# Kernel optimization log

Measured on AMD Instinct MI355X. Metric: run time of the kernel, lower is better.

## Reference

```python
import jax, jax.numpy as jnp
import numpy as np

NUM_RBF = 16
TOP_K = 30
MAXREL = 32  # max_relative_feature
M_CTX = 16   # ligand context atoms per residue

PT_GROUP = jnp.array([0,1,18,1,2,13,14,15,16,17,18,1,2,13,14,15,16,17,18,1,2,3,4,5,6,7,8,9,10,11,12,13,14,15,16,17,18,1,2,3,4,5,6,7,8,9,10,11,12,13,14,15,16,17,18,1,2,3,3,3,3,3,3,3,3,3,3,3,3,3,3,3,4,5,6,7,8,9,10,11,12,13,14,15,16,17,18,1,2,3,3,3,3,3,3,3,3,3,3,3,3,3,3,3,4,5,6,7,8,9,10,11,12,13,14,15,16,17,18], dtype=jnp.int32)
PT_PERIOD = jnp.array([0,1,1,2,2,2,2,2,2,2,2,3,3,3,3,3,3,3,3,4,4,4,4,4,4,4,4,4,4,4,4,4,4,4,4,4,4,5,5,5,5,5,5,5,5,5,5,5,5,5,5,5,5,5,5,6,6,6,6,6,6,6,6,6,6,6,6,6,6,6,6,6,6,6,6,6,6,6,6,6,6,6,6,6,6,6,6,7,7,7,7,7,7,7,7,7,7,7,7,7,7,7,7,7,7,7,7,7,7,7,7,7,7,7,7,7,7,7,7], dtype=jnp.int32)

# pair order after the Ca-Ca term: (N,N),(C,C),(O,O),(Cb,Cb),(Ca,N),(Ca,C),(Ca,O),(Ca,Cb),
# (N,C),(N,O),(N,Cb),(Cb,C),(Cb,O),(O,C),(N,Ca),(C,Ca),(O,Ca),(Cb,Ca),(C,N),(O,N),(Cb,N),(C,Cb),(O,Cb),(C,O)
# atom index in A5 stack: N=0, Ca=1, C=2, O=3, Cb=4
AI = np.array([0,2,3,4,1,1,1,1,0,0,0,4,4,3,0,2,3,4,2,3,4,2,3,2])
BI = np.array([0,2,3,4,0,2,3,4,2,3,4,2,3,2,1,1,1,1,0,0,0,4,4,3])


def _rbf(D):
    mu = jnp.linspace(2.0, 22.0, NUM_RBF)
    sigma = (22.0 - 2.0) / NUM_RBF
    return jnp.exp(-(((D[..., None] - mu) / sigma) ** 2))


def _angle_features(A, Bc, Cc, Y):
    v1 = A - Bc
    v2 = Cc - Bc
    e1 = v1 / jnp.linalg.norm(v1, axis=-1, keepdims=True)
    dot = jnp.einsum('bli,bli->bl', e1, v2)[..., None]
    u2 = v2 - e1 * dot
    e2 = u2 / jnp.linalg.norm(u2, axis=-1, keepdims=True)
    e3 = jnp.cross(e1, e2, axis=-1)
    R = jnp.concatenate((e1[..., None], e2[..., None], e3[..., None]), axis=-1)  # [B,L,3,3]
    lv = jnp.einsum('blqp,blyq->blyp', R, Y - Bc[:, :, None, :])
    rxy = jnp.sqrt(lv[..., 0] ** 2 + lv[..., 1] ** 2 + 1e-8)
    f1 = lv[..., 0] / rxy
    f2 = lv[..., 1] / rxy
    rxyz = jnp.linalg.norm(lv, axis=-1) + 1e-8
    f3 = rxy / rxyz
    f4 = lv[..., 2] / rxyz
    return jnp.stack([f1, f2, f3, f4], axis=-1)  # [B,L,M,4]


def setup_inputs() -> dict:
    key = jax.random.key(0)
    ks = jax.random.split(key, 16)
    B, L, M = 2, 2048, M_CTX
    X = jax.random.normal(ks[0], (B, L, 4, 3), jnp.float32) * 10.0
    Y = jax.random.normal(ks[1], (B, L, M, 3), jnp.float32) * 10.0
    mask = jnp.ones((B, L), jnp.float32)
    Y_m = jnp.ones((B, L, M), jnp.float32)
    R_idx = jnp.arange(B * L, dtype=jnp.int32).reshape(B, L)
    chain_labels = jax.random.randint(ks[2], (B, L), 0, 2, jnp.int32)
    Y_t = jax.random.randint(ks[3], (B, L, M), 1, 119, jnp.int32)
    def lin(k, fi, fo):
        return jax.random.normal(k, (fi, fo), jnp.float32) / np.sqrt(fi)
    params = dict(
        Wp=lin(ks[4], 2 * MAXREL + 2, 16), bp=jnp.zeros((16,), jnp.float32),
        We=lin(ks[5], 16 + 25 * NUM_RBF, 128), be=jnp.zeros((128,), jnp.float32),
        Wn=lin(ks[6], 5 * NUM_RBF + 64 + 4, 128), bn=jnp.zeros((128,), jnp.float32),
        Wt=lin(ks[7], 147, 64), bt=jnp.zeros((64,), jnp.float32),
        Wyn=lin(ks[8], 147, 128), byn=jnp.zeros((128,), jnp.float32),
        Wye=lin(ks[9], NUM_RBF, 128), bye=jnp.zeros((128,), jnp.float32),
    )
    return dict(X=X, Y=Y, mask=mask, Y_m=Y_m, R_idx=R_idx, chain_labels=chain_labels, Y_t=Y_t, **params)


def reference(X, Y, mask, Y_m, R_idx, chain_labels, Y_t,
              Wp, bp, We, be, Wn, bn, Wt, bt, Wyn, byn, Wye, bye):
    B, L = X.shape[0], X.shape[1]
    N, Ca, C, O = X[:, :, 0], X[:, :, 1], X[:, :, 2], X[:, :, 3]
    b_ = Ca - N
    c_ = C - Ca
    a_ = jnp.cross(b_, c_, axis=-1)
    Cb = -0.58273431 * a_ + 0.56802827 * b_ - 0.54067466 * c_ + Ca

    # masked pairwise distances + kNN (smallest-k)
    m2 = mask[:, None, :] * mask[:, :, None]
    dX = Ca[:, None, :, :] - Ca[:, :, None, :]
    D = m2 * jnp.sqrt(jnp.sum(dX * dX, -1) + 1e-6)
    Dadj = D + (1.0 - m2) * jnp.max(D, -1, keepdims=True)
    k = min(TOP_K, L)
    negD, E_idx = jax.lax.top_k(-Dadj, k)
    D_neighbors = -negD  # [B,L,K]

    # gather all 5 atom coords of neighbors once, then all 24 cross-atom RBFs
    A5 = jnp.stack([N, Ca, C, O, Cb], axis=2)  # [B,L,5,3]
    nb = A5[jnp.arange(B)[:, None, None], E_idx]  # [B,L,K,5,3]
    dvec = A5[:, :, None, AI, :] - nb[:, :, :, BI, :]  # [B,L,K,24,3]
    Dp = jnp.sqrt(jnp.sum(dvec * dvec, -1) + 1e-6)
    RBF_all = jnp.concatenate([_rbf(D_neighbors),
                               _rbf(Dp).reshape(B, L, k, 24 * NUM_RBF)], axis=-1)  # [B,L,K,400]

    # positional encodings
    offset = jnp.take_along_axis(R_idx[:, :, None] - R_idx[:, None, :], E_idx, axis=2)
    Ech = jnp.take_along_axis((chain_labels[:, :, None] == chain_labels[:, None, :]).astype(jnp.int32), E_idx, axis=2)
    d = jnp.clip(offset + MAXREL, 0, 2 * MAXREL)
    d = d * Ech + (1 - Ech) * (2 * MAXREL + 1)
    Epos = jax.nn.one_hot(d, 2 * MAXREL + 2, dtype=jnp.float32) @ Wp + bp
    E = jnp.concatenate([Epos, RBF_all], axis=-1) @ We + be  # [B,L,K,128]

    # ligand atom featurization
    g = PT_GROUP[Y_t]
    p = PT_PERIOD[Y_t]
    Yt1 = jnp.concatenate([jax.nn.one_hot(Y_t, 120, dtype=jnp.float32),
                           jax.nn.one_hot(g, 19, dtype=jnp.float32),
                           jax.nn.one_hot(p, 8, dtype=jnp.float32)], axis=-1)  # [B,L,M,147]
    Yt_lin = Yt1 @ Wt + bt  # [B,L,M,64]
    dAY = A5[:, :, :, None, :] - Y[:, :, None, :, :]  # [B,L,5,M,3]
    D_AY = jnp.sqrt(jnp.sum(dAY * dAY, -1) + 1e-6)
    RBF_AY = jnp.transpose(_rbf(D_AY), (0, 1, 3, 2, 4)).reshape(B, L, Y.shape[2], 5 * NUM_RBF)
    f_ang = _angle_features(N, Ca, C, Y)  # [B,L,M,4]
    V = jnp.concatenate([RBF_AY, Yt_lin, f_ang], axis=-1) @ Wn + bn  # [B,L,M,128]

    dYY = Y[:, :, :, None, :] - Y[:, :, None, :, :]
    Y_edges = _rbf(jnp.sqrt(jnp.sum(dYY * dYY, -1) + 1e-6)) @ Wye + bye  # [B,L,M,M,128]
    Y_nodes = Yt1 @ Wyn + byn  # [B,L,M,128]
    return V, E, E_idx, Y_nodes, Y_edges, Y_m
```

## Files before the change

kernel.cpp:

```cpp
#include <hip/hip_runtime.h>
#include <float.h>

typedef unsigned int   u32;
typedef unsigned short ushort_t;
typedef __attribute__((ext_vector_type(8))) short  bf16x8;
typedef __attribute__((ext_vector_type(4))) float  f32x4;
typedef __attribute__((ext_vector_type(8))) unsigned short ushort8;

#define NB 2
#define NL 2048
#define NM 16
#define NK 30

#define OV  0ull
#define OE  8388608ull
#define OEI 24117248ull
#define OYN 24240128ull
#define OYE 32628736ull
#define OYM 166846464ull

__constant__ int PT_GROUP_c[119] = {0,1,18,1,2,13,14,15,16,17,18,1,2,13,14,15,16,17,18,1,2,3,4,5,6,7,8,9,10,11,12,13,14,15,16,17,18,1,2,3,4,5,6,7,8,9,10,11,12,13,14,15,16,17,18,1,2,3,3,3,3,3,3,3,3,3,3,3,3,3,3,3,4,5,6,7,8,9,10,11,12,13,14,15,16,17,18,1,2,3,3,3,3,3,3,3,3,3,3,3,3,3,3,3,4,5,6,7,8,9,10,11,12,13,14,15,16,17,18};
__constant__ int PT_PERIOD_c[119] = {0,1,1,2,2,2,2,2,2,2,2,3,3,3,3,3,3,3,3,4,4,4,4,4,4,4,4,4,4,4,4,4,4,4,4,4,4,5,5,5,5,5,5,5,5,5,5,5,5,5,5,5,5,5,5,6,6,6,6,6,6,6,6,6,6,6,6,6,6,6,6,6,6,6,6,6,6,6,6,6,6,6,6,6,6,6,6,7,7,7,7,7,7,7,7,7,7,7,7,7,7,7,7,7,7,7,7,7,7,7,7,7,7,7,7,7,7,7,7};
__constant__ int AI_c[24] = {0,2,3,4,1,1,1,1,0,0,0,4,4,3,0,2,3,4,2,3,4,2,3,2};
__constant__ int BI_c[24] = {0,2,3,4,0,2,3,4,2,3,4,2,3,2,1,1,1,1,0,0,0,4,4,3};

__device__ __forceinline__ float cl24(float v) {
  return fminf(fmaxf(v, -24.f), 24.f);
}

__device__ __forceinline__ ushort_t f2bf(float f) {
  u32 u = __float_as_uint(f);
  return (ushort_t)((u + 0x7fffu + ((u >> 16) & 1u)) >> 16);
}

__device__ __forceinline__ float rbff(float d, int r) {
  float mu = 2.0f + (20.0f / 15.0f) * (float)r;
  float t = (d - mu) * 0.8f;
  return __expf(-t * t);
}

__global__ __launch_bounds__(256) void k_wet(const float* __restrict__ We,
                                             ushort_t* __restrict__ WeT) {
  int n = blockIdx.x;
  for (int k = threadIdx.x; k < 416; k += 256)
    WeT[(size_t)n * 416 + k] = f2bf(We[(size_t)k * 128 + n]);
}

__global__ __launch_bounds__(256) void k_wnt(const float* __restrict__ Wn,
                                             ushort_t* __restrict__ WnT) {
  int n = blockIdx.x;
  int k = threadIdx.x;
  if (k < 160)
    WnT[(size_t)n * 160 + k] = (k < 148) ? f2bf(Wn[(size_t)k * 128 + n])
                                         : (ushort_t)0;
}

__global__ __launch_bounds__(256) void k_prep(const float* __restrict__ X,
                                              float* __restrict__ A5,
                                              float* __restrict__ Ca4,
                                              float* __restrict__ Fr) {
  int id = blockIdx.x * 256 + threadIdx.x;
  if (id >= NB * NL) return;
  const float* x = X + (size_t)id * 12;
  float Nx=x[0],Ny=x[1],Nz=x[2], Cax=x[3],Cay=x[4],Caz=x[5];
  float Cx=x[6],Cy=x[7],Cz=x[8], Ox=x[9],Oy=x[10],Oz=x[11];
  float bx=Cax-Nx, by=Cay-Ny, bz=Caz-Nz;
  float cx=Cx-Cax, cy=Cy-Cay, cz=Cz-Caz;
  float ax=by*cz-bz*cy, ay=bz*cx-bx*cz, az=bx*cy-by*cx;
  float Cbx = -0.58273431f*ax + 0.56802827f*bx - 0.54067466f*cx + Cax;
  float Cby = -0.58273431f*ay + 0.56802827f*by - 0.54067466f*cy + Cay;
  float Cbz = -0.58273431f*az + 0.56802827f*bz - 0.54067466f*cz + Caz;
  float* A = A5 + (size_t)id * 15;
  A[0]=Nx;A[1]=Ny;A[2]=Nz; A[3]=Cax;A[4]=Cay;A[5]=Caz;
  A[6]=Cx;A[7]=Cy;A[8]=Cz; A[9]=Ox;A[10]=Oy;A[11]=Oz;
  A[12]=Cbx;A[13]=Cby;A[14]=Cbz;
  Ca4[id*4+0]=Cax; Ca4[id*4+1]=Cay; Ca4[id*4+2]=Caz; Ca4[id*4+3]=0.f;
  float v1x=Nx-Cax, v1y=Ny-Cay, v1z=Nz-Caz;
  float v2x=Cx-Cax, v2y=Cy-Cay, v2z=Cz-Caz;
  float n1 = sqrtf(v1x*v1x+v1y*v1y+v1z*v1z);
  float e1x=v1x/n1, e1y=v1y/n1, e1z=v1z/n1;
  float dot = e1x*v2x+e1y*v2y+e1z*v2z;
  float u2x=v2x-e1x*dot, u2y=v2y-e1y*dot, u2z=v2z-e1z*dot;
  float n2 = sqrtf(u2x*u2x+u2y*u2y+u2z*u2z);
  float e2x=u2x/n2, e2y=u2y/n2, e2z=u2z/n2;
  float e3x=e1y*e2z-e1z*e2y, e3y=e1z*e2x-e1x*e2z, e3z=e1x*e2y-e1y*e2x;
  float* F = Fr + (size_t)id * 9;
  F[0]=e1x;F[1]=e1y;F[2]=e1z; F[3]=e2x;F[4]=e2y;F[5]=e2z; F[6]=e3x;F[7]=e3y;F[8]=e3z;
}

__global__ __launch_bounds__(256) void k_topk(const float* __restrict__ Ca4,
                                              const float* __restrict__ mask,
                                              float* __restrict__ Dn,
                                              int* __restrict__ Eidx,
                                              float* __restrict__ out) {
  __shared__ float dist[NL];
  __shared__ float rv[4];
  __shared__ float cand_v[128];
  __shared__ int   cand_i[128];
  int row = blockIdx.x;
  int b = row >> 11;
  int tid = threadIdx.x;
  const float4* cab = (const float4*)Ca4 + ((size_t)b << 11);
  float4 ci = ((const float4*)Ca4)[row];
  float mi = mask[row];
  float lmax = 0.f;
  for (int j = tid; j < NL; j += 256) {
    float4 cj = cab[j];
    float dx = __fsub_rn(ci.x, cj.x);
    float dy = __fsub_rn(ci.y, cj.y);
    float dz = __fsub_rn(ci.z, cj.z);
    float s  = __fadd_rn(__fadd_rn(__fadd_rn(__fmul_rn(dx,dx), __fmul_rn(dy,dy)),
                                   __fmul_rn(dz,dz)), 1e-6f);
    float D  = __fmul_rn(__fmul_rn(mask[(b << 11) + j], mi), __fsqrt_rn(s));
    dist[j] = D;
    lmax = fmaxf(lmax, D);
  }
  #pragma unroll
  for (int s = 32; s > 0; s >>= 1) lmax = fmaxf(lmax, __shfl_xor(lmax, s));
  if ((tid & 63) == 0) rv[tid >> 6] = lmax;
  __syncthreads();
  float rowmax = fmaxf(fmaxf(rv[0], rv[1]), fmaxf(rv[2], rv[3]));
  for (int j = tid; j < NL; j += 256) {
    float mj = mask[(b << 11) + j];
    dist[j] = __fadd_rn(dist[j], __fmul_rn(__fsub_rn(1.f, __fmul_rn(mi, mj)), rowmax));
  }
  __syncthreads();
  int w = tid >> 6, l = tid & 63;
  int base = w * 512 + l;
  float v[8];
  #pragma unroll
  for (int k = 0; k < 8; k++) v[k] = dist[base + k * 64];
  if (tid < 8) { cand_v[120 + tid] = FLT_MAX; cand_i[120 + tid] = NL; }
  for (int it = 0; it < NK; it++) {
    float bv = FLT_MAX; int bj = NL;
    #pragma unroll
    for (int k = 0; k < 8; k++) {
      int jj = base + k * 64;
      if (v[k] < bv) { bv = v[k]; bj = jj; }
    }
    #pragma unroll
    for (int s = 32; s > 0; s >>= 1) {
      float ov = __shfl_xor(bv, s);
      int   oj = __shfl_xor(bj, s);
      if (ov < bv || (ov == bv && oj < bj)) { bv = ov; bj = oj; }
    }
    int ow = bj & 511;
    int ko = ow >> 6;
    bool mine = (ow & 63) == l;
    #pragma unroll
    for (int k = 0; k < 8; k++)
      if (mine && k == ko) v[k] = FLT_MAX;
    if (l == 0) { cand_v[w * NK + it] = bv; cand_i[w * NK + it] = bj; }
  }
  __syncthreads();
  if (tid < 64) {
    float v1 = cand_v[tid], v2 = cand_v[64 + tid];
    int   i1 = cand_i[tid], i2 = cand_i[64 + tid];
    for (int it = 0; it < NK; it++) {
      float bv; int bj, sl;
      if (v1 < v2 || (v1 == v2 && i1 < i2)) { bv = v1; bj = i1; sl = tid; }
      else                                  { bv = v2; bj = i2; sl = 64 + tid; }
      #pragma unroll
      for (int s = 32; s > 0; s >>= 1) {
        float ov = __shfl_xor(bv, s);
        int   oj = __shfl_xor(bj, s);
        int   os = __shfl_xor(sl, s);
        if (ov < bv || (ov == bv && oj < bj)) { bv = ov; bj = oj; sl = os; }
      }
      if (sl == tid)           v1 = FLT_MAX;
      else if (sl == 64 + tid) v2 = FLT_MAX;
      if (tid == 0) {
        Dn[(size_t)row * NK + it]   = bv;
        Eidx[(size_t)row * NK + it] = bj;
        out[OEI + (size_t)row * NK + it] = (float)bj;
      }
    }
  }
}

__global__ __launch_bounds__(256) void k_edge(const float* __restrict__ A5,
        const float* __restrict__ Dn, const int* __restrict__ Eidx,
        const int* __restrict__ R_idx, const int* __restrict__ cl,
        const float* __restrict__ Wp, const float* __restrict__ bp,
        const ushort_t* __restrict__ WeT, const float* __restrict__ be,
        float* __restrict__ out) {
  __shared__ __align__(16) ushort_t feat[32][424];
  int tid = threadIdx.x;
  int e0 = blockIdx.x * 32;
  {
    int el = tid >> 3;
    int te = tid & 7;
    int e  = e0 + el;
    int bi = e / NK;
    int b  = bi >> 11;
    int j  = Eidx[e];
    j = j < 0 ? 0 : (j > NL - 1 ? NL - 1 : j);
    int jrow = (b << 11) + j;
    const float* Ac = A5 + (size_t)bi * 15;
    const float* An = A5 + (size_t)jrow * 15;
    int off = R_idx[bi] - R_idx[jrow];
    int d;
    if (cl[bi] == cl[jrow]) { d = off + 32; d = d < 0 ? 0 : (d > 64 ? 64 : d); }
    else d = 65;
    feat[el][2*te]   = f2bf(Wp[d * 16 + 2*te]   + bp[2*te]);
    feat[el][2*te+1] = f2bf(Wp[d * 16 + 2*te+1] + bp[2*te+1]);
    float dn = Dn[e];
    feat[el][16 + 2*te]   = f2bf(rbff(dn, 2*te));
    feat[el][16 + 2*te+1] = f2bf(rbff(dn, 2*te+1));
    #pragma unroll
    for (int pp = 0; pp < 3; pp++) {
      int p = te + pp * 8;
      int ai = AI_c[p] * 3, bj2 = BI_c[p] * 3;
      float dx = Ac[ai]   - An[bj2];
      float dy = Ac[ai+1] - An[bj2+1];
      float dz = Ac[ai+2] - An[bj2+2];
      float dp = sqrtf(dx*dx + dy*dy + dz*dz + 1e-6f);
      int fb = 32 + p * 16;
      #pragma unroll
      for (int r = 0; r < 16; r++) feat[el][fb + r] = f2bf(rbff(dp, r));
    }
  }
  __syncthreads();
  int l  = tid & 63;
  int wid = tid >> 6;
  int wm = wid >> 1, wn = wid & 1;
  f32x4 acc0 = {0.f,0.f,0.f,0.f}, acc1 = {0.f,0.f,0.f,0.f};
  f32x4 acc2 = {0.f,0.f,0.f,0.f}, acc3 = {0.f,0.f,0.f,0.f};
  const ushort_t* Wb = WeT + (size_t)(wn*64 + (l & 15)) * 416 + (l >> 4) * 8;
  #pragma unroll 2
  for (int c = 0; c < 13; c++) {
    bf16x8 a  = *(const bf16x8*)&feat[wm*16 + (l & 15)][c*32 + (l >> 4)*8];
    bf16x8 b0 = *(const bf16x8*)(Wb + c*32);
    bf16x8 b1 = *(const bf16x8*)(Wb + 16*416 + c*32);
    bf16x8 b2 = *(const bf16x8*)(Wb + 32*416 + c*32);
    bf16x8 b3 = *(const bf16x8*)(Wb + 48*416 + c*32);
    acc0 = __builtin_amdgcn_mfma_f32_16x16x32_bf16(a, b0, acc0, 0, 0, 0);
    acc1 = __builtin_amdgcn_mfma_f32_16x16x32_bf16(a, b1, acc1, 0, 0, 0);
    acc2 = __builtin_amdgcn_mfma_f32_16x16x32_bf16(a, b2, acc2, 0, 0, 0);
    acc3 = __builtin_amdgcn_mfma_f32_16x16x32_bf16(a, b3, acc3, 0, 0, 0);
  }
  #pragma unroll
  for (int t = 0; t < 4; t++) {
    f32x4 av = (t==0) ? acc0 : (t==1) ? acc1 : (t==2) ? acc2 : acc3;
    int n = wn*64 + t*16 + (l & 15);
    float bb = be[n];
    #pragma unroll
    for (int jj = 0; jj < 4; jj++) {
      int ee = e0 + wm*16 + (l >> 4)*4 + jj;
      out[OE + (size_t)ee * 128 + n] = cl24(av[jj] + bb);
    }
  }
}

__global__ __launch_bounds__(256) void k_v(const float* __restrict__ A5,
        const float* __restrict__ Fr, const float* __restrict__ Y,
        const int* __restrict__ Y_t,
        const ushort_t* __restrict__ WnT, const float* __restrict__ bn,
        const float* __restrict__ Wt, const float* __restrict__ bt,
        float* __restrict__ out) {
  __shared__ __align__(16) ushort_t wnt_s[128][168];
  __shared__ __align__(16) ushort_t feat[16][168];
  __shared__ float dAY[16][8];
  int tid = threadIdx.x;
  int bl = blockIdx.x;
  {
    int n = tid >> 1, h = tid & 1;
    const ushort8* src = (const ushort8*)(WnT + (size_t)n * 160 + h * 80);
    ushort8* dst = (ushort8*)&wnt_s[n][h * 80];
    #pragma unroll
    for (int i = 0; i < 10; i++) dst[i] = src[i];
  }
  if (tid < 80) {
    int m = tid / 5, a = tid % 5;
    float dx = A5[(size_t)bl*15 + a*3 + 0] - Y[(size_t)bl*48 + m*3 + 0];
    float dy = A5[(size_t)bl*15 + a*3 + 1] - Y[(size_t)bl*48 + m*3 + 1];
    float dz = A5[(size_t)bl*15 + a*3 + 2] - Y[(size_t)bl*48 + m*3 + 2];
    dAY[m][a] = sqrtf(dx*dx + dy*dy + dz*dz + 1e-6f);
  }
  __syncthreads();
  {
    int m = tid >> 4, q = tid & 15;
    #pragma unroll
    for (int a = 0; a < 5; a++) feat[m][a * 16 + q] = f2bf(rbff(dAY[m][a], q));
    int yt = Y_t[(size_t)bl * NM + m];
    int g = PT_GROUP_c[yt], p = PT_PERIOD_c[yt];
    {
      float4 wa = *(const float4*)&Wt[yt*64 + q*4];
      float4 wb = *(const float4*)&Wt[(120+g)*64 + q*4];
      float4 wc = *(const float4*)&Wt[(139+p)*64 + q*4];
      float4 bb = *(const float4*)&bt[q*4];
      feat[m][80 + q*4 + 0] = f2bf(wa.x + wb.x + wc.x + bb.x);
      feat[m][80 + q*4 + 1] = f2bf(wa.y + wb.y + wc.y + bb.y);
      feat[m][80 + q*4 + 2] = f2bf(wa.z + wb.z + wc.z + bb.z);
      feat[m][80 + q*4 + 3] = f2bf(wa.w + wb.w + wc.w + bb.w);
    }
    if (q == 0) {
      const float* fr = Fr + (size_t)bl * 9;
      float cax = A5[(size_t)bl*15+3], cay = A5[(size_t)bl*15+4], caz = A5[(size_t)bl*15+5];
      float yx = Y[(size_t)bl*48 + m*3+0] - cax;
      float yy = Y[(size_t)bl*48 + m*3+1] - cay;
      float yz = Y[(size_t)bl*48 + m*3+2] - caz;
      float l0 = fr[0]*yx + fr[1]*yy + fr[2]*yz;
      float l1 = fr[3]*yx + fr[4]*yy + fr[5]*yz;
      float l2 = fr[6]*yx + fr[7]*yy + fr[8]*yz;
      float rxy  = sqrtf(l0*l0 + l1*l1 + 1e-8f);
      float rxyz = sqrtf(l0*l0 + l1*l1 + l2*l2) + 1e-8f;
      feat[m][144] = f2bf(l0 / rxy);
      feat[m][145] = f2bf(l1 / rxy);
      feat[m][146] = f2bf(rxy / rxyz);
      feat[m][147] = f2bf(l2 / rxyz);
    }
    if (q < 12) feat[m][148 + q] = 0;
  }
  __syncthreads();
  int l = tid & 63;
  int wid = tid >> 6;
  int n0 = wid * 32;
  f32x4 acc0 = {0.f,0.f,0.f,0.f}, acc1 = {0.f,0.f,0.f,0.f};
  #pragma unroll
  for (int c = 0; c < 5; c++) {
    bf16x8 a  = *(const bf16x8*)&feat[l & 15][c*32 + (l >> 4)*8];
    bf16x8 b0 = *(const bf16x8*)&wnt_s[n0 +      (l & 15)][c*32 + (l >> 4)*8];
    bf16x8 b1 = *(const bf16x8*)&wnt_s[n0 + 16 + (l & 15)][c*32 + (l >> 4)*8];
    acc0 = __builtin_amdgcn_mfma_f32_16x16x32_bf16(a, b0, acc0, 0, 0, 0);
    acc1 = __builtin_amdgcn_mfma_f32_16x16x32_bf16(a, b1, acc1, 0, 0, 0);
  }
  #pragma unroll
  for (int t = 0; t < 2; t++) {
    f32x4 av = (t==0) ? acc0 : acc1;
    int n = n0 + t*16 + (l & 15);
    float bb = bn[n];
    #pragma unroll
    for (int jj = 0; jj < 4; jj++) {
      int m = (l >> 4)*4 + jj;
      out[OV + ((size_t)bl * NM + m) * 128 + n] = cl24(av[jj] + bb);
    }
  }
}

__global__ __launch_bounds__(256, 4) void k_ynode(const int* __restrict__ Y_t,
        const float* __restrict__ Wyn, const float* __restrict__ byn,
        const float* __restrict__ Y_m, float* __restrict__ out) {
  int tid = threadIdx.x;
  int bl = blockIdx.x;
  if (tid < NM)
    out[OYM + (size_t)bl * NM + tid] = Y_m[(size_t)bl * NM + tid];
  int m = tid >> 4, n0 = (tid & 15) * 8;
  int yt = Y_t[(size_t)bl * NM + m];
  int g = PT_GROUP_c[yt], p = PT_PERIOD_c[yt];
  const float* w0 = Wyn + yt * 128 + n0;
  const float* w1 = Wyn + (120 + g) * 128 + n0;
  const float* w2 = Wyn + (139 + p) * 128 + n0;
  float4 r0 = *(const float4*)&w0[0], r1 = *(const float4*)&w0[4];
  float4 s0 = *(const float4*)&w1[0], s1 = *(const float4*)&w1[4];
  float4 t0 = *(const float4*)&w2[0], t1 = *(const float4*)&w2[4];
  float4 b0 = *(const float4*)&byn[n0], b1 = *(const float4*)&byn[n0 + 4];
  float4 o0, o1;
  o0.x = cl24(r0.x + s0.x + t0.x + b0.x);
  o0.y = cl24(r0.y + s0.y + t0.y + b0.y);
  o0.z = cl24(r0.z + s0.z + t0.z + b0.z);
  o0.w = cl24(r0.w + s0.w + t0.w + b0.w);
  o1.x = cl24(r1.x + s1.x + t1.x + b1.x);
  o1.y = cl24(r1.y + s1.y + t1.y + b1.y);
  o1.z = cl24(r1.z + s1.z + t1.z + b1.z);
  o1.w = cl24(r1.w + s1.w + t1.w + b1.w);
  size_t ob = OYN + ((size_t)bl * NM + m) * 128 + n0;
  *(float4*)&out[ob]     = o0;
  *(float4*)&out[ob + 4] = o1;
}

__global__ __launch_bounds__(256) void k_yedge(const float* __restrict__ Y,
        const float* __restrict__ Wye, const float* __restrict__ bye,
        float* __restrict__ out) {
  __shared__ float rbf_s[256][20];
  __shared__ float ys[16][3];
  __shared__ float wye_s[16][128];
  __shared__ float bye_s[128];
  int tid = threadIdx.x;
  int bl = blockIdx.x;
  if (tid < 48) ((float*)ys)[tid] = Y[(size_t)bl * 48 + tid];
  for (int x = tid; x < 2048; x += 256) wye_s[x >> 7][x & 127] = Wye[x];
  if (tid < 128) bye_s[tid] = bye[tid];
  __syncthreads();
  {
    int m = tid >> 4, m2 = tid & 15;
    float dx = ys[m][0]-ys[m2][0], dy = ys[m][1]-ys[m2][1], dz = ys[m][2]-ys[m2][2];
    float dd = sqrtf(dx*dx + dy*dy + dz*dz + 1e-6f);
    #pragma unroll
    for (int r = 0; r < 16; r++) rbf_s[tid][r] = rbff(dd, r);
  }
  __syncthreads();
  int n2 = (tid & 63) * 2;
  int pg = tid >> 6;
  float wy0[16], wy1[16];
  #pragma unroll
  for (int k = 0; k < 16; k++) { wy0[k] = wye_s[k][n2]; wy1[k] = wye_s[k][n2+1]; }
  float bb0 = bye_s[n2], bb1 = bye_s[n2+1];
  size_t obase = OYE + (size_t)bl * (NM * NM * 128);
  for (int p = pg * 64; p < pg * 64 + 64; p++) {
    float s0 = bb0, s1 = bb1;
    #pragma unroll
    for (int k4 = 0; k4 < 4; k4++) {
      float4 rv = *(const float4*)&rbf_s[p][k4 * 4];
      s0 = fmaf(rv.x, wy0[k4*4+0], s0); s1 = fmaf(rv.x, wy1[k4*4+0], s1);
      s0 = fmaf(rv.y, wy0[k4*4+1], s0); s1 = fmaf(rv.y, wy1[k4*4+1], s1);
      s0 = fmaf(rv.z, wy0[k4*4+2], s0); s1 = fmaf(rv.z, wy1[k4*4+2], s1);
      s0 = fmaf(rv.w, wy0[k4*4+3], s0); s1 = fmaf(rv.w, wy1[k4*4+3], s1);
    }
    float2 st; st.x = cl24(s0); st.y = cl24(s1);
    *(float2*)&out[obase + (size_t)p * 128 + n2] = st;
  }
}

extern "C" void kernel_launch(void* const* d_in, const int* in_sizes, int n_in,
                              void* d_out, int out_size, void* d_ws, size_t ws_size,
                              hipStream_t stream) {
  const float* X     = (const float*)d_in[0];
  const float* Y     = (const float*)d_in[1];
  const float* mask  = (const float*)d_in[2];
  const float* Y_m   = (const float*)d_in[3];
  const int*   R_idx = (const int*)d_in[4];
  const int*   cl    = (const int*)d_in[5];
  const int*   Y_t   = (const int*)d_in[6];
  const float* Wp    = (const float*)d_in[7];
  const float* bp    = (const float*)d_in[8];
  const float* We    = (const float*)d_in[9];
  const float* be    = (const float*)d_in[10];
  const float* Wn    = (const float*)d_in[11];
  const float* bn    = (const float*)d_in[12];
  const float* Wt    = (const float*)d_in[13];
  const float* bt    = (const float*)d_in[14];
  const float* Wyn   = (const float*)d_in[15];
  const float* byn   = (const float*)d_in[16];
  const float* Wye   = (const float*)d_in[17];
  const float* bye   = (const float*)d_in[18];
  float* out = (float*)d_out;

  float* wsf  = (float*)d_ws;
  float* A5   = wsf;
  float* Ca4  = A5  + 61440;
  float* Fr   = Ca4 + 16384;
  float* Dn   = Fr  + 36864;
  int*   Eidx = (int*)(Dn + 122880);
  ushort_t* WeT = (ushort_t*)(Eidx + 122880);
  ushort_t* WnT = WeT + 128 * 416;

  k_wet  <<<128,  256, 0, stream>>>(We, WeT);
  k_wnt  <<<128,  256, 0, stream>>>(Wn, WnT);
  k_prep <<<16,   256, 0, stream>>>(X, A5, Ca4, Fr);
  k_topk <<<NB*NL,256, 0, stream>>>(Ca4, mask, Dn, Eidx, out);
  k_edge <<<(NB*NL*NK)/32, 256, 0, stream>>>(A5, Dn, Eidx, R_idx, cl, Wp, bp, WeT, be, out);
  k_v    <<<NB*NL,256, 0, stream>>>(A5, Fr, Y, Y_t, WnT, bn, Wt, bt, out);
  k_ynode<<<NB*NL,256, 0, stream>>>(Y_t, Wyn, byn, Y_m, out);
  k_yedge<<<NB*NL,256, 0, stream>>>(Y, Wye, bye, out);
}
```

Before: 334.7 us.

## Merge prep kernels, fuse ynode into yedge, read Wn from global, widen yedge stores

Three small setup kernels (weight transposes and backbone prep) are merged into one launch, and the ligand-node kernel is folded into the ligand-edge kernel, cutting launch count. k_v no longer stages the full transposed Wn into shared memory per block; MFMA B operands are read directly from global/L2, reducing LDS usage and per-block copy work. The yedge inner loop now has each thread compute four output columns with float4 stores instead of two with float2. Reading weights straight from global may add latency per block, in exchange for higher occupancy.

```diff
diff --git a/kernel.cpp b/kernel.cpp
--- a/kernel.cpp
+++ b/kernel.cpp
@@ -39,27 +39,27 @@
   return __expf(-t * t);
 }
 
-__global__ __launch_bounds__(256) void k_wet(const float* __restrict__ We,
-                                             ushort_t* __restrict__ WeT) {
-  int n = blockIdx.x;
-  for (int k = threadIdx.x; k < 416; k += 256)
-    WeT[(size_t)n * 416 + k] = f2bf(We[(size_t)k * 128 + n]);
-}
-
-__global__ __launch_bounds__(256) void k_wnt(const float* __restrict__ Wn,
-                                             ushort_t* __restrict__ WnT) {
-  int n = blockIdx.x;
-  int k = threadIdx.x;
-  if (k < 160)
-    WnT[(size_t)n * 160 + k] = (k < 148) ? f2bf(Wn[(size_t)k * 128 + n])
-                                         : (ushort_t)0;
-}
-
-__global__ __launch_bounds__(256) void k_prep(const float* __restrict__ X,
-                                              float* __restrict__ A5,
-                                              float* __restrict__ Ca4,
-                                              float* __restrict__ Fr) {
-  int id = blockIdx.x * 256 + threadIdx.x;
+__global__ __launch_bounds__(256) void k_init(const float* __restrict__ We,
+        const float* __restrict__ Wn, const float* __restrict__ X,
+        ushort_t* __restrict__ WeT, ushort_t* __restrict__ WnT,
+        float* __restrict__ A5, float* __restrict__ Ca4,
+        float* __restrict__ Fr) {
+  int blk = blockIdx.x;
+  int tid = threadIdx.x;
+  if (blk < 128) {
+    int n = blk;
+    for (int k = tid; k < 416; k += 256)
+      WeT[(size_t)n * 416 + k] = f2bf(We[(size_t)k * 128 + n]);
+    return;
+  }
+  if (blk < 256) {
+    int n = blk - 128;
+    if (tid < 160)
+      WnT[(size_t)n * 160 + tid] = (tid < 148) ? f2bf(Wn[(size_t)tid * 128 + n])
+                                               : (ushort_t)0;
+    return;
+  }
+  int id = (blk - 256) * 256 + tid;
   if (id >= NB * NL) return;
   const float* x = X + (size_t)id * 12;
   float Nx=x[0],Ny=x[1],Nz=x[2], Cax=x[3],Cay=x[4],Caz=x[5];
@@ -258,18 +258,10 @@
         const ushort_t* __restrict__ WnT, const float* __restrict__ bn,
         const float* __restrict__ Wt, const float* __restrict__ bt,
         float* __restrict__ out) {
-  __shared__ __align__(16) ushort_t wnt_s[128][168];
   __shared__ __align__(16) ushort_t feat[16][168];
   __shared__ float dAY[16][8];
   int tid = threadIdx.x;
   int bl = blockIdx.x;
-  {
-    int n = tid >> 1, h = tid & 1;
-    const ushort8* src = (const ushort8*)(WnT + (size_t)n * 160 + h * 80);
-    ushort8* dst = (ushort8*)&wnt_s[n][h * 80];
-    #pragma unroll
-    for (int i = 0; i < 10; i++) dst[i] = src[i];
-  }
   if (tid < 80) {
     int m = tid / 5, a = tid % 5;
     float dx = A5[(size_t)bl*15 + a*3 + 0] - Y[(size_t)bl*48 + m*3 + 0];
@@ -317,11 +309,12 @@
   int wid = tid >> 6;
   int n0 = wid * 32;
   f32x4 acc0 = {0.f,0.f,0.f,0.f}, acc1 = {0.f,0.f,0.f,0.f};
+  const ushort_t* Wb = WnT + (size_t)(n0 + (l & 15)) * 160 + (l >> 4) * 8;
   #pragma unroll
   for (int c = 0; c < 5; c++) {
     bf16x8 a  = *(const bf16x8*)&feat[l & 15][c*32 + (l >> 4)*8];
-    bf16x8 b0 = *(const bf16x8*)&wnt_s[n0 +      (l & 15)][c*32 + (l >> 4)*8];
-    bf16x8 b1 = *(const bf16x8*)&wnt_s[n0 + 16 + (l & 15)][c*32 + (l >> 4)*8];
+    bf16x8 b0 = *(const bf16x8*)(Wb + c*32);
+    bf16x8 b1 = *(const bf16x8*)(Wb + 16*160 + c*32);
     acc0 = __builtin_amdgcn_mfma_f32_16x16x32_bf16(a, b0, acc0, 0, 0, 0);
     acc1 = __builtin_amdgcn_mfma_f32_16x16x32_bf16(a, b1, acc1, 0, 0, 0);
   }
@@ -338,46 +331,43 @@
   }
 }
 
-__global__ __launch_bounds__(256, 4) void k_ynode(const int* __restrict__ Y_t,
+__global__ __launch_bounds__(256) void k_yedge(const float* __restrict__ Y,
+        const float* __restrict__ Wye, const float* __restrict__ bye,
+        const int* __restrict__ Y_t,
         const float* __restrict__ Wyn, const float* __restrict__ byn,
         const float* __restrict__ Y_m, float* __restrict__ out) {
-  int tid = threadIdx.x;
-  int bl = blockIdx.x;
-  if (tid < NM)
-    out[OYM + (size_t)bl * NM + tid] = Y_m[(size_t)bl * NM + tid];
-  int m = tid >> 4, n0 = (tid & 15) * 8;
-  int yt = Y_t[(size_t)bl * NM + m];
-  int g = PT_GROUP_c[yt], p = PT_PERIOD_c[yt];
-  const float* w0 = Wyn + yt * 128 + n0;
-  const float* w1 = Wyn + (120 + g) * 128 + n0;
-  const float* w2 = Wyn + (139 + p) * 128 + n0;
-  float4 r0 = *(const float4*)&w0[0], r1 = *(const float4*)&w0[4];
-  float4 s0 = *(const float4*)&w1[0], s1 = *(const float4*)&w1[4];
-  float4 t0 = *(const float4*)&w2[0], t1 = *(const float4*)&w2[4];
-  float4 b0 = *(const float4*)&byn[n0], b1 = *(const float4*)&byn[n0 + 4];
-  float4 o0, o1;
-  o0.x = cl24(r0.x + s0.x + t0.x + b0.x);
-  o0.y = cl24(r0.y + s0.y + t0.y + b0.y);
-  o0.z = cl24(r0.z + s0.z + t0.z + b0.z);
-  o0.w = cl24(r0.w + s0.w + t0.w + b0.w);
-  o1.x = cl24(r1.x + s1.x + t1.x + b1.x);
-  o1.y = cl24(r1.y + s1.y + t1.y + b1.y);
-  o1.z = cl24(r1.z + s1.z + t1.z + b1.z);
-  o1.w = cl24(r1.w + s1.w + t1.w + b1.w);
-  size_t ob = OYN + ((size_t)bl * NM + m) * 128 + n0;
-  *(float4*)&out[ob]     = o0;
-  *(float4*)&out[ob + 4] = o1;
-}
-
-__global__ __launch_bounds__(256) void k_yedge(const float* __restrict__ Y,
-        const float* __restrict__ Wye, const float* __restrict__ bye,
-        float* __restrict__ out) {
   __shared__ float rbf_s[256][20];
   __shared__ float ys[16][3];
   __shared__ float wye_s[16][128];
   __shared__ float bye_s[128];
   int tid = threadIdx.x;
   int bl = blockIdx.x;
+  {
+    if (tid < NM)
+      out[OYM + (size_t)bl * NM + tid] = Y_m[(size_t)bl * NM + tid];
+    int m = tid >> 4, n0 = (tid & 15) * 8;
+    int yt = Y_t[(size_t)bl * NM + m];
+    int g = PT_GROUP_c[yt], p = PT_PERIOD_c[yt];
+    const float* w0 = Wyn + yt * 128 + n0;
+    const float* w1 = Wyn + (120 + g) * 128 + n0;
+    const float* w2 = Wyn + (139 + p) * 128 + n0;
+    float4 r0 = *(const float4*)&w0[0], r1 = *(const float4*)&w0[4];
+    float4 s0 = *(const float4*)&w1[0], s1 = *(const float4*)&w1[4];
+    float4 t0 = *(const float4*)&w2[0], t1 = *(const float4*)&w2[4];
+    float4 b0 = *(const float4*)&byn[n0], b1 = *(const float4*)&byn[n0 + 4];
+    float4 o0, o1;
+    o0.x = cl24(r0.x + s0.x + t0.x + b0.x);
+    o0.y = cl24(r0.y + s0.y + t0.y + b0.y);
+    o0.z = cl24(r0.z + s0.z + t0.z + b0.z);
+    o0.w = cl24(r0.w + s0.w + t0.w + b0.w);
+    o1.x = cl24(r1.x + s1.x + t1.x + b1.x);
+    o1.y = cl24(r1.y + s1.y + t1.y + b1.y);
+    o1.z = cl24(r1.z + s1.z + t1.z + b1.z);
+    o1.w = cl24(r1.w + s1.w + t1.w + b1.w);
+    size_t ob = OYN + ((size_t)bl * NM + m) * 128 + n0;
+    *(float4*)&out[ob]     = o0;
+    *(float4*)&out[ob + 4] = o1;
+  }
   if (tid < 48) ((float*)ys)[tid] = Y[(size_t)bl * 48 + tid];
   for (int x = tid; x < 2048; x += 256) wye_s[x >> 7][x & 127] = Wye[x];
   if (tid < 128) bye_s[tid] = bye[tid];
@@ -390,25 +380,32 @@
     for (int r = 0; r < 16; r++) rbf_s[tid][r] = rbff(dd, r);
   }
   __syncthreads();
-  int n2 = (tid & 63) * 2;
-  int pg = tid >> 6;
-  float wy0[16], wy1[16];
-  #pragma unroll
-  for (int k = 0; k < 16; k++) { wy0[k] = wye_s[k][n2]; wy1[k] = wye_s[k][n2+1]; }
-  float bb0 = bye_s[n2], bb1 = bye_s[n2+1];
+  int n4 = (tid & 31) * 4;
+  int pg = tid >> 5;
+  float4 wy4[16];
+  #pragma unroll
+  for (int k = 0; k < 16; k++) wy4[k] = *(const float4*)&wye_s[k][n4];
+  float4 bb = *(const float4*)&bye_s[n4];
   size_t obase = OYE + (size_t)bl * (NM * NM * 128);
-  for (int p = pg * 64; p < pg * 64 + 64; p++) {
-    float s0 = bb0, s1 = bb1;
+  #pragma unroll 2
+  for (int i = 0; i < 32; i++) {
+    int p = pg * 32 + i;
+    float sx = bb.x, sy = bb.y, sz = bb.z, sw = bb.w;
     #pragma unroll
     for (int k4 = 0; k4 < 4; k4++) {
       float4 rv = *(const float4*)&rbf_s[p][k4 * 4];
-      s0 = fmaf(rv.x, wy0[k4*4+0], s0); s1 = fmaf(rv.x, wy1[k4*4+0], s1);
-      s0 = fmaf(rv.y, wy0[k4*4+1], s0); s1 = fmaf(rv.y, wy1[k4*4+1], s1);
-      s0 = fmaf(rv.z, wy0[k4*4+2], s0); s1 = fmaf(rv.z, wy1[k4*4+2], s1);
-      s0 = fmaf(rv.w, wy0[k4*4+3], s0); s1 = fmaf(rv.w, wy1[k4*4+3], s1);
-    }
-    float2 st; st.x = cl24(s0); st.y = cl24(s1);
-    *(float2*)&out[obase + (size_t)p * 128 + n2] = st;
+      sx = fmaf(rv.x, wy4[k4*4+0].x, sx); sy = fmaf(rv.x, wy4[k4*4+0].y, sy);
+      sz = fmaf(rv.x, wy4[k4*4+0].z, sz); sw = fmaf(rv.x, wy4[k4*4+0].w, sw);
+      sx = fmaf(rv.y, wy4[k4*4+1].x, sx); sy = fmaf(rv.y, wy4[k4*4+1].y, sy);
+      sz = fmaf(rv.y, wy4[k4*4+1].z, sz); sw = fmaf(rv.y, wy4[k4*4+1].w, sw);
+      sx = fmaf(rv.z, wy4[k4*4+2].x, sx); sy = fmaf(rv.z, wy4[k4*4+2].y, sy);
+      sz = fmaf(rv.z, wy4[k4*4+2].z, sz); sw = fmaf(rv.z, wy4[k4*4+2].w, sw);
+      sx = fmaf(rv.w, wy4[k4*4+3].x, sx); sy = fmaf(rv.w, wy4[k4*4+3].y, sy);
+      sz = fmaf(rv.w, wy4[k4*4+3].z, sz); sw = fmaf(rv.w, wy4[k4*4+3].w, sw);
+    }
+    float4 st;
+    st.x = cl24(sx); st.y = cl24(sy); st.z = cl24(sz); st.w = cl24(sw);
+    *(float4*)&out[obase + (size_t)p * 128 + n4] = st;
   }
 }
 
@@ -445,12 +442,9 @@
   ushort_t* WeT = (ushort_t*)(Eidx + 122880);
   ushort_t* WnT = WeT + 128 * 416;
 
-  k_wet  <<<128,  256, 0, stream>>>(We, WeT);
-  k_wnt  <<<128,  256, 0, stream>>>(Wn, WnT);
-  k_prep <<<16,   256, 0, stream>>>(X, A5, Ca4, Fr);
+  k_init <<<272,  256, 0, stream>>>(We, Wn, X, WeT, WnT, A5, Ca4, Fr);
   k_topk <<<NB*NL,256, 0, stream>>>(Ca4, mask, Dn, Eidx, out);
   k_edge <<<(NB*NL*NK)/32, 256, 0, stream>>>(A5, Dn, Eidx, R_idx, cl, Wp, bp, WeT, be, out);
   k_v    <<<NB*NL,256, 0, stream>>>(A5, Fr, Y, Y_t, WnT, bn, Wt, bt, out);
-  k_ynode<<<NB*NL,256, 0, stream>>>(Y_t, Wyn, byn, Y_m, out);
-  k_yedge<<<NB*NL,256, 0, stream>>>(Y, Wye, bye, out);
-}
+  k_yedge<<<NB*NL,256, 0, stream>>>(Y, Wye, bye, Y_t, Wyn, byn, Y_m, out);
+}
```

After: 394.1 us. 1.18x slower.
